# Kernel tuning notes

Hardware: AMD Instinct MI355X
Metric: run time of the kernel (lower is better)

Reference implementation:

```python
import jax, jax.numpy as jnp
import numpy as np

N = 100000   # nodes
E = 1600000  # edges
G = 1000     # graphs
S = 32       # state_dim
H = 128      # hidden_dim_message / hidden_dim_output
F = 1        # num_features (edge coulomb)
ROUNDS = 5
NEG_SLOPE = 0.01
LN_EPS = 1e-5


def _ln(x, g, b):
    m = jnp.mean(x, axis=-1, keepdims=True)
    v = jnp.var(x, axis=-1, keepdims=True)
    return (x - m) / jnp.sqrt(v + LN_EPS) * g + b


def _lrelu(x):
    return jnp.where(x >= 0, x, NEG_SLOPE * x)


def _kaiming(k, shape):
    # torch kaiming_normal_(mode='fan_out', nonlinearity='leaky_relu'); W stored [in,out]
    gain = np.sqrt(2.0 / (1.0 + NEG_SLOPE ** 2))
    std = gain / np.sqrt(shape[1])
    return jax.random.normal(k, shape, dtype=jnp.float32) * std


def setup_inputs() -> dict:
    key = jax.random.key(0)
    ks = jax.random.split(key, 10)
    return {
        'node_from': jax.random.randint(ks[0], (E,), 0, N),
        'node_to': jax.random.randint(ks[1], (E,), 0, N),
        'edge_coulomb': jax.random.normal(ks[2], (E, F), dtype=jnp.float32),
        'node_graph_index': jax.random.randint(ks[3], (N,), 0, G),
        'num_nodes': N,
        'num_graphs': G,
        # message_net params
        'W1': _kaiming(ks[4], (S + F, H)), 'b1': jnp.zeros((H,), jnp.float32),
        'g1': jnp.ones((H,), jnp.float32), 'be1': jnp.zeros((H,), jnp.float32),
        'W2': _kaiming(ks[5], (H, S)), 'b2': jnp.zeros((S,), jnp.float32),
        'g2': jnp.ones((S,), jnp.float32), 'be2': jnp.zeros((S,), jnp.float32),
        # output_net params
        'Wo1': _kaiming(ks[6], (S, H)), 'bo1': jnp.zeros((H,), jnp.float32),
        'go': jnp.ones((H,), jnp.float32), 'beo': jnp.zeros((H,), jnp.float32),
        'Wo2': _kaiming(ks[7], (H, 2)), 'bo2': jnp.zeros((2,), jnp.float32),
    }


def reference(node_from, node_to, edge_coulomb, node_graph_index, num_nodes, num_graphs,
              W1, b1, g1, be1, W2, b2, g2, be2, Wo1, bo1, go, beo, Wo2, bo2):
    state = jnp.zeros((num_nodes, S), dtype=edge_coulomb.dtype)
    for _ in range(ROUNDS):
        inp = jnp.concatenate([state[node_from], edge_coulomb], axis=1)  # [E, S+F]
        h = _lrelu(_ln(inp @ W1 + b1, g1, be1))                           # [E, H]
        msg = _lrelu(_ln(h @ W2 + b2, g2, be2))                           # [E, S]
        state = state + jax.ops.segment_sum(msg, node_to, num_segments=num_nodes)
    graph_state = jax.ops.segment_sum(state, node_graph_index, num_segments=num_graphs)  # [G, S]
    h = _lrelu(_ln(graph_state @ Wo1 + bo1, go, beo))
    ev = h @ Wo2 + bo2                                                    # [G, 2]
    mu = ev[:, :1]
    var = jax.nn.softplus(ev[:, 1:])
    return jnp.concatenate([mu, var], axis=1)
```

## Files before the change

### kernel.cpp

```cpp
#include <hip/hip_runtime.h>
#include <hip/hip_bf16.h>

#define NN 100000
#define NE 1600000
#define NG 1000
#define SS 32
#define HH 128
#define ROUNDS 5

constexpr float NEG = 0.01f;
constexpr float EPS = 1e-5f;

constexpr long al4(long x)  { return (x + 3) & ~3L; }
constexpr long al16(long x) { return (x + 15) & ~15L; }

constexpr long OFF_STATE = 0;
constexpr long OFF_GS    = OFF_STATE + (long)NN * SS;
constexpr long OFF_W1T   = OFF_GS + (long)NG * SS;
constexpr long OFF_B1    = OFF_W1T + HH * 33;
constexpr long OFF_G1    = OFF_B1 + HH;
constexpr long OFF_BE1   = OFF_G1 + HH;
constexpr long OFF_W2    = OFF_BE1 + HH;
constexpr long OFF_B2    = OFF_W2 + HH * SS;
constexpr long OFF_G2    = OFF_B2 + SS;
constexpr long OFF_BE2   = OFF_G2 + SS;
constexpr long OFF_WO1   = OFF_BE2 + SS;
constexpr long OFF_BO1   = OFF_WO1 + SS * HH;
constexpr long OFF_GO    = OFF_BO1 + HH;
constexpr long OFF_BEO   = OFF_GO + HH;
constexpr long OFF_WO2   = OFF_BEO + HH;
constexpr long OFF_BO2   = OFF_WO2 + HH * 2;
constexpr long OFF_W1L   = al4(OFF_BO2 + 2);
constexpr long OFF_WSC   = OFF_W1L + HH;
constexpr long OFF_W1B   = al4(OFF_WSC + 2);
constexpr long OFF_W2F   = OFF_W1B + 2048;
constexpr long OFF_WPK   = OFF_W2F + 2048;
constexpr long OFF_Z0P   = OFF_WPK + 192;
constexpr long W_END     = OFF_Z0P + 68;
constexpr long OFF_DELTA = al4(W_END);
constexpr long F_Z      = al4(W_END);
constexpr long F_START  = al4(F_Z + (long)NN * 68);
constexpr long F_CURSOR = F_START + NN + 4;
constexpr long F_SSTART = F_CURSOR + NN;
constexpr long F_SCUR   = F_SSTART + NN + 4;
constexpr long F_BSUM   = F_SCUR + NN;
constexpr long F_GDEG   = F_BSUM + 512;
constexpr long F_GSTART = F_GDEG + NG;
constexpr long F_GCUR   = F_GSTART + NG + 4;
constexpr long F_GLIST  = F_GCUR + NG;
constexpr long F_EPK    = al16(F_GLIST + NN);
constexpr long F_SP     = F_EPK + (long)NE * 2;
constexpr long F_MSG    = al16(F_SP + NE);
constexpr long F_RC     = F_MSG;
constexpr long WS_TOTAL = F_MSG + (long)NE * 16;
constexpr long WS_FALLBACK = OFF_DELTA + (long)NN * SS;
constexpr int  NBLK_N  = (NN + 255) / 256;
constexpr int  CHSHIFT_E = 19;
constexpr int  NCH_E     = (NE + (1 << CHSHIFT_E) - 1) >> CHSHIFT_E;
constexpr int  CHSHIFT_P = 20;
constexpr int  NCH_P     = (NE + (1 << CHSHIFT_P) - 1) >> CHSHIFT_P;

typedef float f32x4 __attribute__((ext_vector_type(4)));
typedef unsigned int u32x4 __attribute__((ext_vector_type(4)));
typedef short s16x8 __attribute__((ext_vector_type(8)));

__device__ __forceinline__ s16x8 as_s16x8(u32x4 u) {
    union { u32x4 a; s16x8 b; } c; c.a = u; return c.b;
}
__device__ __forceinline__ float bf2f(unsigned short u) {
    union { unsigned int i; float f; } v;
    v.i = ((unsigned int)u) << 16;
    return v.f;
}
__device__ __forceinline__ float lo_bf(unsigned int p) {
    union { unsigned int i; float f; } v; v.i = p << 16; return v.f;
}
__device__ __forceinline__ float hi_bf(unsigned int p) {
    union { unsigned int i; float f; } v; v.i = p & 0xFFFF0000u; return v.f;
}
__device__ __forceinline__ unsigned short f2bf(float f) {
    union { float f; unsigned int u; } x; x.f = f;
    return (unsigned short)((x.u + 0x7FFFu + ((x.u >> 16) & 1u)) >> 16);
}
__device__ __forceinline__ unsigned int pack_bf2(float a, float b) {
    return (unsigned int)f2bf(a) | ((unsigned int)f2bf(b) << 16);
}
#if defined(__has_builtin)
#if __has_builtin(__builtin_amdgcn_cvt_pk_bf16_f32)
#define HAVE_CVT_PK_BF16 1
#endif
#endif
__device__ __forceinline__ unsigned int cvt2bf(float a, float b) {
#ifdef HAVE_CVT_PK_BF16
    auto r = __builtin_amdgcn_cvt_pk_bf16_f32(a, b);
    unsigned int u; __builtin_memcpy(&u, &r, 4); return u;
#else
    return pack_bf2(a, b);
#endif
}
template <int CTRL>
__device__ __forceinline__ float ror_add(float x) {
    int v = __builtin_amdgcn_update_dpp(0, __float_as_int(x), CTRL, 0xF, 0xF, true);
    return x + __int_as_float(v);
}
__device__ __forceinline__ float row_reduce16(float x) {
    x = ror_add<0x121>(x);
    x = ror_add<0x122>(x);
    x = ror_add<0x124>(x);
    x = ror_add<0x128>(x);
    return x;
}
__device__ __forceinline__ int is_bf16(const void* g1raw) {
    return (((const unsigned int*)g1raw)[0] & 0xFFFFu) != 0u;
}
__device__ __forceinline__ float ldf(const void* p, long idx, int bf) {
    return bf ? bf2f(((const unsigned short*)p)[idx]) : ((const float*)p)[idx];
}

__global__ void prep_kernel(
    const void* __restrict__ W1,  const void* __restrict__ b1,
    const void* __restrict__ g1,  const void* __restrict__ be1,
    const void* __restrict__ W2,  const void* __restrict__ b2,
    const void* __restrict__ g2,  const void* __restrict__ be2,
    const void* __restrict__ Wo1, const void* __restrict__ bo1,
    const void* __restrict__ go,  const void* __restrict__ beo,
    const void* __restrict__ Wo2, const void* __restrict__ bo2,
    float* __restrict__ ws)
{
    const int bf = is_bf16(g1);
    long idx = (long)blockIdx.x * blockDim.x + threadIdx.x;
    if (idx < (long)NN * SS) { ws[OFF_STATE + idx] = 0.f; ws[OFF_DELTA + idx] = 0.f; }
    if (idx < (long)NG * SS) ws[OFF_GS + idx] = 0.f;
    if (idx < NN) { ((int*)(ws + F_CURSOR))[idx] = 0; ((int*)(ws + F_SCUR))[idx] = 0; }
    if (idx < NG) ((int*)(ws + F_GDEG))[idx] = 0;
    if (idx < 33 * HH) {
        int i = (int)(idx / HH), k = (int)(idx % HH);
        ws[OFF_W1T + (long)k * 33 + i] = ldf(W1, idx, bf);
    }
    if (idx < HH) {
        ws[OFF_B1  + idx] = ldf(b1,  idx, bf);
        ws[OFF_G1  + idx] = ldf(g1,  idx, bf);
        ws[OFF_BE1 + idx] = ldf(be1, idx, bf);
        ws[OFF_BO1 + idx] = ldf(bo1, idx, bf);
        ws[OFF_GO  + idx] = ldf(go,  idx, bf);
        ws[OFF_BEO + idx] = ldf(beo, idx, bf);
        ws[OFF_W1L + idx] = ldf(W1, (long)32 * HH + idx, bf);
    }
    if (idx == 0) {
        float sw = 0.f, sq = 0.f;
        float sb = 0.f, qb = 0.f, db = 0.f;
        for (int i = 0; i < HH; i++) {
            float w = ldf(W1, (long)32 * HH + i, bf);
            float x = ldf(b1, i, bf);
            sw += w; sq = fmaf(w, w, sq);
            sb += x; qb = fmaf(x, x, qb); db = fmaf(x, w, db);
        }
        ws[OFF_WSC] = sw; ws[OFF_WSC + 1] = sq;
        float* z0s = ws + OFF_Z0P + 64;
        z0s[0] = sb; z0s[1] = qb; z0s[2] = db; z0s[3] = 0.f;
    }
    if (idx < 64) {
        ((unsigned int*)(ws + OFF_Z0P))[idx] =
            cvt2bf(ldf(b1, 2 * idx, bf), ldf(b1, 2 * idx + 1, bf));
    }
    if (idx < HH * SS) ws[OFF_W2 + idx] = ldf(W2, idx, bf);
    if (idx < SS) {
        ws[OFF_B2  + idx] = ldf(b2,  idx, bf);
        ws[OFF_G2  + idx] = ldf(g2,  idx, bf);
        ws[OFF_BE2 + idx] = ldf(be2, idx, bf);
    }
    if (idx < SS * HH) ws[OFF_WO1 + idx] = ldf(Wo1, idx, bf);
    if (idx < HH * 2)  ws[OFF_WO2 + idx] = ldf(Wo2, idx, bf);
    if (idx < 2)       ws[OFF_BO2 + idx] = ldf(bo2, idx, bf);
    if (idx < 2048) {
        int w = (int)idx;
        int qq = w & 3, L = (w >> 2) & 63, t = (int)(w >> 8);
        int k0 = (L >> 4) * 8 + 2 * qq;
        int n  = t * 16 + (L & 15);
        ((unsigned int*)(ws + OFF_W1B))[w] =
            pack_bf2(ldf(W1, (long)k0 * HH + n, bf), ldf(W1, (long)(k0 + 1) * HH + n, bf));
    }
    if (idx < 2048) {
        int w = (int)idx;
        int qq = w & 3, L = (w >> 2) & 63, t2 = (w >> 8) & 1, ks = (int)(w >> 9);
        int k0 = ks * 32 + (L >> 4) * 8 + 2 * qq;
        int n  = t2 * 16 + (L & 15);
        float v0 = ldf(W2, (long)k0 * SS + n, bf);
        float v1 = ldf(W2, (long)(k0 + 1) * SS + n, bf);
        ((unsigned int*)(ws + OFF_W2F))[w] = pack_bf2(v0, v1);
    }
    if (idx < 192) {
        int w = (int)idx;
        int grp = w / 12, rem = w % 12, slot = rem >> 2, q = rem & 3;
        int ks = grp >> 2, quad = grp & 3;
        int n = ks * 32 + quad * 8 + 2 * q;
        float v0, v1;
        if (slot == 0)      { v0 = ldf(W1, (long)32 * HH + n, bf); v1 = ldf(W1, (long)32 * HH + n + 1, bf); }
        else if (slot == 1) { v0 = ldf(g1, n, bf);  v1 = ldf(g1, n + 1, bf); }
        else                { v0 = ldf(be1, n, bf); v1 = ldf(be1, n + 1, bf); }
        ((unsigned int*)(ws + OFF_WPK))[w] = pack_bf2(v0, v1);
    }
}

__global__ void fillseq_kernel(const int* __restrict__ nfrom, const int* __restrict__ nto,
                               const void* __restrict__ ec, const void* __restrict__ g1raw,
                               float* ws) {
    int e = blockIdx.x * 256 + threadIdx.x;
    if (e < NE) {
        int u = nfrom[e];
        int v = nto[e];
        float ecv = ldf(ec, e, is_bf16(g1raw));
        int drank = atomicAdd(&((int*)(ws + F_CURSOR))[v], 1);
        int srank = atomicAdd(&((int*)(ws + F_SCUR))[u], 1);
        union { float f; unsigned int i; } c; c.f = ecv;
        u32x4 o; o[0] = (unsigned int)u; o[1] = c.i; o[2] = (unsigned int)drank; o[3] = (unsigned int)srank;
        *(u32x4*)((unsigned int*)(ws + F_RC) + (long)e * 4) = o;
    }
}

__global__ void scan1_kernel(float* ws, long degOff, long startOff) {
    __shared__ int sh[256];
    int* deg   = (int*)(ws + degOff);
    int* start = (int*)(ws + startOff);
    int* bsum  = (int*)(ws + F_BSUM);
    int i = blockIdx.x * 256 + threadIdx.x;
    int x = (i < NN) ? deg[i] : 0;
    sh[threadIdx.x] = x;
    __syncthreads();
    for (int off = 1; off < 256; off <<= 1) {
        int t = (threadIdx.x >= off) ? sh[threadIdx.x - off] : 0;
        __syncthreads();
        sh[threadIdx.x] += t;
        __syncthreads();
    }
    int incl = sh[threadIdx.x];
    if (i < NN) start[i] = incl - x;
    if (threadIdx.x == 255) bsum[blockIdx.x] = incl;
}

__global__ void scan2p_kernel(float* ws) {
    __shared__ int sh[512];
    int* bsum = (int*)(ws + F_BSUM);
    int t = threadIdx.x;
    int x = (t < NBLK_N) ? bsum[t] : 0;
    sh[t] = x;
    __syncthreads();
    for (int off = 1; off < 512; off <<= 1) {
        int v = (t >= off) ? sh[t - off] : 0;
        __syncthreads();
        sh[t] += v;
        __syncthreads();
    }
    if (t < NBLK_N) bsum[t] = sh[t] - x;
}

__global__ void scan3_kernel(float* ws, long startOff) {
    int* start  = (int*)(ws + startOff);
    int* bsum   = (int*)(ws + F_BSUM);
    int i = blockIdx.x * 256 + threadIdx.x;
    if (i < NN) {
        start[i] += bsum[i >> 8];
        if (i == 0) start[NN] = NE;
    }
}

__global__ void epkc_kernel(float* ws, int chunk) {
    int e = blockIdx.x * 256 + threadIdx.x;
    if (e < NE) {
        u32x4 rc = *(const u32x4*)((const unsigned int*)(ws + F_RC) + (long)e * 4);
        int spos = ((const int*)(ws + F_SSTART))[rc[0]] + (int)rc[3];
        if ((spos >> CHSHIFT_E) == chunk) {
            uint2 o; o.x = rc[0]; o.y = rc[1];
            *(uint2*)((unsigned int*)(ws + F_EPK) + (long)spos * 2) = o;
        }
    }
}

__global__ void spc_kernel(const int* __restrict__ nto, float* ws, int chunk) {
    int e = blockIdx.x * 256 + threadIdx.x;
    if (e < NE) {
        u32x4 rc = *(const u32x4*)((const unsigned int*)(ws + F_RC) + (long)e * 4);
        int dpos = ((const int*)(ws + F_START))[nto[e]] + (int)rc[2];
        if ((dpos >> CHSHIFT_P) == chunk) {
            int spos = ((const int*)(ws + F_SSTART))[rc[0]] + (int)rc[3];
            ((int*)(ws + F_SP))[dpos] = spos;
        }
    }
}

__global__ void ghist_kernel(const int* __restrict__ gidx, float* ws) {
    int i = blockIdx.x * 256 + threadIdx.x;
    if (i < NN) atomicAdd(&((int*)(ws + F_GDEG))[gidx[i]], 1);
}

__global__ void gscan_kernel(float* ws) {
    __shared__ int sh[1024];
    int* deg   = (int*)(ws + F_GDEG);
    int* start = (int*)(ws + F_GSTART);
    int* cur   = (int*)(ws + F_GCUR);
    int t = threadIdx.x;
    int x = (t < NG) ? deg[t] : 0;
    sh[t] = x;
    __syncthreads();
    for (int off = 1; off < 1024; off <<= 1) {
        int v = (t >= off) ? sh[t - off] : 0;
        __syncthreads();
        sh[t] += v;
        __syncthreads();
    }
    if (t < NG) { start[t] = sh[t] - x; cur[t] = sh[t] - x; }
    if (t == 0) start[NG] = NN;
}

__global__ void gfill_kernel(const int* __restrict__ gidx, float* ws) {
    int i = blockIdx.x * 256 + threadIdx.x;
    if (i < NN) {
        int pos = atomicAdd(&((int*)(ws + F_GCUR))[gidx[i]], 1);
        ((int*)(ws + F_GLIST))[pos] = i;
    }
}

__global__ void z0_kernel(float* __restrict__ ws)
{
    long idx = (long)blockIdx.x * 256 + threadIdx.x;
    if (idx < (long)NN * 68) {
        int slot = (int)(idx % 68);
        ((unsigned int*)(ws + F_Z))[idx] = ((const unsigned int*)(ws + OFF_Z0P))[slot];
    }
}

__launch_bounds__(256)
__global__ void node_kernel(float* __restrict__ ws, int do_z)
{
    __shared__ unsigned short zl[4][16 * 136];
    __shared__ float stl[64 * 33];
    const long nbase = (long)blockIdx.x * 64;

    {
        int t = threadIdx.x;
        int vl = t >> 2, sub = t & 3;
        long v = nbase + vl;
        if (v < NN) {
            const int* start = (const int*)(ws + F_START);
            const int* SPp   = (const int*)(ws + F_SP);
            const u32x4* mb = (const u32x4*)(ws + F_MSG);
            int s0 = start[v], s1 = start[v + 1];
            float* st = ws + OFF_STATE + v * SS + sub * 8;
            float a0 = st[0], a1 = st[1], a2 = st[2], a3 = st[3];
            float a4 = st[4], a5 = st[5], a6 = st[6], a7 = st[7];
            int p = s0;
            for (; p + 3 < s1; p += 4) {
                int q0 = SPp[p], q1 = SPp[p + 1], q2 = SPp[p + 2], q3 = SPp[p + 3];
                u32x4 m0 = mb[(long)q0 * 4 + sub];
                u32x4 m1 = mb[(long)q1 * 4 + sub];
                u32x4 m2 = mb[(long)q2 * 4 + sub];
                u32x4 m3 = mb[(long)q3 * 4 + sub];
                a0 += lo_bf(m0[0]); a1 += hi_bf(m0[0]);
                a2 += lo_bf(m0[1]); a3 += hi_bf(m0[1]);
                a4 += lo_bf(m0[2]); a5 += hi_bf(m0[2]);
                a6 += lo_bf(m0[3]); a7 += hi_bf(m0[3]);
                a0 += lo_bf(m1[0]); a1 += hi_bf(m1[0]);
                a2 += lo_bf(m1[1]); a3 += hi_bf(m1[1]);
                a4 += lo_bf(m1[2]); a5 += hi_bf(m1[2]);
                a6 += lo_bf(m1[3]); a7 += hi_bf(m1[3]);
                a0 += lo_bf(m2[0]); a1 += hi_bf(m2[0]);
                a2 += lo_bf(m2[1]); a3 += hi_bf(m2[1]);
                a4 += lo_bf(m2[2]); a5 += hi_bf(m2[2]);
                a6 += lo_bf(m2[3]); a7 += hi_bf(m2[3]);
                a0 += lo_bf(m3[0]); a1 += hi_bf(m3[0]);
                a2 += lo_bf(m3[1]); a3 += hi_bf(m3[1]);
                a4 += lo_bf(m3[2]); a5 += hi_bf(m3[2]);
                a6 += lo_bf(m3[3]); a7 += hi_bf(m3[3]);
            }
            for (; p < s1; ++p) {
                int spv = SPp[p];
                u32x4 m = mb[(long)spv * 4 + sub];
                a0 += lo_bf(m[0]); a1 += hi_bf(m[0]);
                a2 += lo_bf(m[1]); a3 += hi_bf(m[1]);
                a4 += lo_bf(m[2]); a5 += hi_bf(m[2]);
                a6 += lo_bf(m[3]); a7 += hi_bf(m[3]);
            }
            st[0] = a0; st[1] = a1; st[2] = a2; st[3] = a3;
            st[4] = a4; st[5] = a5; st[6] = a6; st[7] = a7;
            float* sl = stl + vl * 33 + sub * 8;
            sl[0] = a0; sl[1] = a1; sl[2] = a2; sl[3] = a3;
            sl[4] = a4; sl[5] = a5; sl[6] = a6; sl[7] = a7;
        }
    }
    if (!do_z) return;
    __syncthreads();

    const int wv = threadIdx.x >> 6, lane = threadIdx.x & 63;
    const int col = lane & 15, quad = lane >> 4;
    const long vbase = nbase + wv * 16;
    if (vbase >= NN) return;

    const float* sl = stl + (wv * 16 + col) * 33 + quad * 8;
    float st[8];
#pragma unroll
    for (int j = 0; j < 8; j++) st[j] = sl[j];

    u32x4 au;
    au[0] = cvt2bf(st[0], st[1]);
    au[1] = cvt2bf(st[2], st[3]);
    au[2] = cvt2bf(st[4], st[5]);
    au[3] = cvt2bf(st[6], st[7]);
    s16x8 af = as_s16x8(au);

    const u32x4* W1B = (const u32x4*)(ws + OFF_W1B);
    const float* B1 = ws + OFF_B1;
    f32x4 acc[8];
#pragma unroll
    for (int t = 0; t < 8; t++) {
        float bb = B1[t * 16 + col];
        acc[t][0] = bb; acc[t][1] = bb; acc[t][2] = bb; acc[t][3] = bb;
        acc[t] = __builtin_amdgcn_mfma_f32_16x16x32_bf16(af, as_s16x8(W1B[t * 64 + lane]), acc[t], 0, 0, 0);
    }

    float s[4] = {0.f, 0.f, 0.f, 0.f}, q[4] = {0.f, 0.f, 0.f, 0.f}, d[4] = {0.f, 0.f, 0.f, 0.f};
    const float* W1L = ws + OFF_W1L;
#pragma unroll
    for (int t = 0; t < 8; t++) {
        float wl = W1L[t * 16 + col];
#pragma unroll
        for (int r = 0; r < 4; r++) {
            float z = acc[t][r];
            s[r] += z; q[r] = fmaf(z, z, q[r]); d[r] = fmaf(z, wl, d[r]);
        }
    }
#pragma unroll
    for (int r = 0; r < 4; r++) {
        float sr = row_reduce16(s[r]);
        float qr = row_reduce16(q[r]);
        float dr = row_reduce16(d[r]);
        if (col == 0) {
            f32x4 o; o[0] = sr; o[1] = qr; o[2] = dr; o[3] = 0.f;
            *(f32x4*)(ws + F_Z + (vbase + quad * 4 + r) * 68 + 64) = o;
        }
    }

    unsigned short* zw_ = zl[wv];
#pragma unroll
    for (int t = 0; t < 8; t++) {
        unsigned int p01 = cvt2bf(acc[t][0], acc[t][1]);
        unsigned int p23 = cvt2bf(acc[t][2], acc[t][3]);
        unsigned short* b = zw_ + quad * (4 * 136) + t * 16 + col;
        b[0]       = (unsigned short)p01;
        b[136]     = (unsigned short)(p01 >> 16);
        b[2 * 136] = (unsigned short)p23;
        b[3 * 136] = (unsigned short)(p23 >> 16);
    }
    unsigned int* zg = (unsigned int*)(ws + F_Z);
#pragma unroll
    for (int it = 0; it < 4; it++) {
        int byte = it * 1024 + lane * 16;
        int node = byte >> 8;
        int ko   = (byte & 255) >> 2;
        u32x4 val = *(const u32x4*)(zw_ + node * 136 + ((byte & 255) >> 1));
        *(u32x4*)(zg + (vbase + node) * 68L + ko) = val;
    }
}

__launch_bounds__(256)
__global__ void edge_src_kernel(float* __restrict__ ws)
{
    const int lane = threadIdx.x & 63, wv = threadIdx.x >> 6;
    const int col = lane & 15, quad = lane >> 4;

    const u32x4* W2Fp = (const u32x4*)(ws + OFF_W2F);
    u32x4 w2f[8];
#pragma unroll
    for (int i = 0; i < 8; i++) w2f[i] = W2Fp[i * 64 + lane];
    u32x4 wlp[4], gp[4], bep[4];
    const u32x4* WPKp = (const u32x4*)(ws + OFF_WPK);
#pragma unroll
    for (int ks = 0; ks < 4; ks++) {
        const u32x4* W = WPKp + (ks * 4 + quad) * 3;
        wlp[ks] = W[0]; gp[ks] = W[1]; bep[ks] = W[2];
    }
    f32x4 g2h[2], be2h[2], b2h[2];
#pragma unroll
    for (int t2 = 0; t2 < 2; t2++) {
        g2h[t2]  = *(const f32x4*)(ws + OFF_G2  + t2 * 16 + quad * 4);
        be2h[t2] = *(const f32x4*)(ws + OFF_BE2 + t2 * 16 + quad * 4);
        b2h[t2]  = *(const f32x4*)(ws + OFF_B2  + t2 * 16 + quad * 4);
    }
    const float sw1 = ws[OFF_WSC], sqw1 = ws[OFF_WSC + 1];

    const uint2* EPKp = (const uint2*)((const unsigned int*)(ws + F_EPK));
    const long tbase = ((long)blockIdx.x * 4 + wv) * 4;

    uint2 epk[4];
#pragma unroll
    for (int k = 0; k < 4; k++)
        epk[k] = EPKp[(tbase + k) * 16 + col];
    f32x4 zst[4];
#pragma unroll
    for (int k = 0; k < 4; k++)
        zst[k] = *(const f32x4*)(ws + F_Z + (long)(int)epk[k].x * 68 + 64);

#pragma unroll
    for (int k = 0; k < 4; k++) {
        const int epos = (int)((tbase + k) * 16) + col;
        const int u = (int)epk[k].x;
        union { unsigned int i; float f; } cc; cc.i = epk[k].y;
        const float ecv = cc.f;

        float sumh = fmaf(ecv, sw1, zst[k][0]);
        float sqh  = fmaf(ecv, fmaf(ecv, sqw1, 2.f * zst[k][2]), zst[k][1]);
        float mean = sumh * (1.f / HH);
        float var  = fmaxf(sqh * (1.f / HH) - mean * mean, 0.f);
        float inv  = rsqrtf(var + EPS);
        const float alpha = inv, beta = -mean * inv;

        const unsigned int* zrow = (const unsigned int*)(ws + F_Z) + (long)u * 68;
        u32x4 zw[4];
#pragma unroll
        for (int ks = 0; ks < 4; ks++)
            zw[ks] = *(const u32x4*)(zrow + ks * 16 + quad * 4);

        f32x4 acc2[2];
        acc2[0] = b2h[0]; acc2[1] = b2h[1];

#pragma unroll
        for (int ks = 0; ks < 4; ks++) {
            u32x4 zwv = zw[ks];
            u32x4 hu;
#pragma unroll
            for (int w = 0; w < 4; w++) {
                float z0 = lo_bf(zwv[w]), z1 = hi_bf(zwv[w]);
                float h0 = fmaf(ecv, lo_bf(wlp[ks][w]), z0);
                float h1 = fmaf(ecv, hi_bf(wlp[ks][w]), z1);
                h0 = fmaf(h0, alpha, beta);
                h1 = fmaf(h1, alpha, beta);
                h0 = fmaf(h0, lo_bf(gp[ks][w]), lo_bf(bep[ks][w]));
                h1 = fmaf(h1, hi_bf(gp[ks][w]), hi_bf(bep[ks][w]));
                h0 = fmaxf(h0, NEG * h0);
                h1 = fmaxf(h1, NEG * h1);
                hu[w] = cvt2bf(h0, h1);
            }
            s16x8 hf = as_s16x8(hu);
            acc2[0] = __builtin_amdgcn_mfma_f32_16x16x32_bf16(as_s16x8(w2f[ks * 2 + 0]), hf, acc2[0], 0, 0, 0);
            acc2[1] = __builtin_amdgcn_mfma_f32_16x16x32_bf16(as_s16x8(w2f[ks * 2 + 1]), hf, acc2[1], 0, 0, 0);
        }

        float s2 = 0.f, q2 = 0.f;
#pragma unroll
        for (int t2 = 0; t2 < 2; t2++)
#pragma unroll
            for (int r = 0; r < 4; r++) { float vv = acc2[t2][r]; s2 += vv; q2 = fmaf(vv, vv, q2); }
        s2 += __shfl_xor(s2, 16); q2 += __shfl_xor(q2, 16);
        s2 += __shfl_xor(s2, 32); q2 += __shfl_xor(q2, 32);
        float mean2 = s2 * (1.f / SS);
        float var2  = fmaxf(q2 * (1.f / SS) - mean2 * mean2, 0.f);
        float inv2  = rsqrtf(var2 + EPS);
        const float a2 = inv2, b2c = -mean2 * inv2;

        unsigned int* dst = (unsigned int*)(ws + F_MSG) + (long)epos * 16;
#pragma unroll
        for (int t2 = 0; t2 < 2; t2++) {
            float m0 = fmaf(fmaf(acc2[t2][0], a2, b2c), g2h[t2][0], be2h[t2][0]);
            float m1 = fmaf(fmaf(acc2[t2][1], a2, b2c), g2h[t2][1], be2h[t2][1]);
            float m2 = fmaf(fmaf(acc2[t2][2], a2, b2c), g2h[t2][2], be2h[t2][2]);
            float m3 = fmaf(fmaf(acc2[t2][3], a2, b2c), g2h[t2][3], be2h[t2][3]);
            m0 = fmaxf(m0, NEG * m0); m1 = fmaxf(m1, NEG * m1);
            m2 = fmaxf(m2, NEG * m2); m3 = fmaxf(m3, NEG * m3);
            uint2 o; o.x = cvt2bf(m0, m1); o.y = cvt2bf(m2, m3);
            *(uint2*)(dst + t2 * 8 + quad * 2) = o;
        }
    }
}

__launch_bounds__(256)
__global__ void graph_gather_kernel(float* __restrict__ ws)
{
    int t = blockIdx.x * 256 + threadIdx.x;
    int g = t >> 5;
    if (g >= NG) return;
    int j = t & 31;
    const int* start = (const int*)(ws + F_GSTART);
    const int* list  = (const int*)(ws + F_GLIST);
    int s0 = start[g], s1 = start[g + 1];
    float acc = 0.f;
    for (int p = s0; p < s1; ++p)
        acc += ws[OFF_STATE + (long)list[p] * SS + j];
    ws[OFF_GS + (long)g * SS + j] = acc;
}

__launch_bounds__(256)
__global__ void edge_atomic_kernel(const int* __restrict__ nfrom, const int* __restrict__ nto,
                                   const void* __restrict__ ec, const void* __restrict__ g1raw,
                                   const float* __restrict__ cws, float* delta)
{
    int e = blockIdx.x * 256 + threadIdx.x;
    if (e >= NE) return;
    const float* state = cws + OFF_STATE;
    const float* W1T = cws + OFF_W1T;
    const float* B1  = cws + OFF_B1;
    const float* G1  = cws + OFF_G1;
    const float* BE1 = cws + OFF_BE1;
    const float* W2  = cws + OFF_W2;
    const float* B2  = cws + OFF_B2;
    const float* G2  = cws + OFF_G2;
    const float* BE2 = cws + OFF_BE2;
    int u = nfrom[e];
    float inp[33];
    const float4* srow = (const float4*)(state + (long)u * SS);
#pragma unroll
    for (int i = 0; i < 8; i++) {
        float4 v = srow[i];
        inp[i * 4 + 0] = v.x; inp[i * 4 + 1] = v.y;
        inp[i * 4 + 2] = v.z; inp[i * 4 + 3] = v.w;
    }
    inp[32] = ldf(ec, e, is_bf16(g1raw));
    float sum = 0.f, sq = 0.f;
    for (int k = 0; k < HH; k++) {
        const float* wr = W1T + k * 33;
        float a = B1[k];
#pragma unroll
        for (int i = 0; i < 33; i++) a = fmaf(inp[i], wr[i], a);
        sum += a; sq = fmaf(a, a, sq);
    }
    float mean = sum * (1.f / HH);
    float var  = sq * (1.f / HH) - mean * mean;
    float inv  = rsqrtf(var + EPS);
    float msg[SS];
#pragma unroll
    for (int j = 0; j < SS; j++) msg[j] = B2[j];
    for (int k = 0; k < HH; k++) {
        const float* wr = W1T + k * 33;
        float a = B1[k];
#pragma unroll
        for (int i = 0; i < 33; i++) a = fmaf(inp[i], wr[i], a);
        float hk = fmaf((a - mean) * inv, G1[k], BE1[k]);
        hk = hk >= 0.f ? hk : NEG * hk;
        const float* w2r = W2 + k * SS;
#pragma unroll
        for (int j = 0; j < SS; j++) msg[j] = fmaf(hk, w2r[j], msg[j]);
    }
    float s2 = 0.f, q2 = 0.f;
#pragma unroll
    for (int j = 0; j < SS; j++) { s2 += msg[j]; q2 = fmaf(msg[j], msg[j], q2); }
    float m2 = s2 * (1.f / SS);
    float v2 = q2 * (1.f / SS) - m2 * m2;
    float i2 = rsqrtf(v2 + EPS);
    int v = nto[e];
    float* drow = delta + (long)v * SS;
#pragma unroll
    for (int j = 0; j < SS; j++) {
        float mj = fmaf((msg[j] - m2) * i2, G2[j], BE2[j]);
        mj = mj >= 0.f ? mj : NEG * mj;
        atomicAdd(drow + j, mj);
    }
}

__global__ void update_kernel(float* ws)
{
    long idx = (long)blockIdx.x * blockDim.x + threadIdx.x;
    if (idx < (long)NN * SS) {
        ws[OFF_STATE + idx] += ws[OFF_DELTA + idx];
        ws[OFF_DELTA + idx] = 0.f;
    }
}

__global__ void graph_kernel(const int* __restrict__ gidx, float* ws)
{
    long idx = (long)blockIdx.x * blockDim.x + threadIdx.x;
    if (idx < (long)NN * SS) {
        int i = (int)(idx >> 5);
        int j = (int)(idx & 31);
        atomicAdd(&ws[OFF_GS + (long)gidx[i] * SS + j], ws[OFF_STATE + idx]);
    }
}

__global__ void readout_kernel(const float* __restrict__ ws, const void* __restrict__ g1raw,
                               void* __restrict__ out)
{
    int g = blockIdx.x;
    int j = threadIdx.x;
    __shared__ float row[SS];
    __shared__ float buf[HH];
    __shared__ float p0[HH];
    __shared__ float p1[HH];

    const float* gs  = ws + OFF_GS;
    const float* Wo1 = ws + OFF_WO1;
    if (j < SS) row[j] = gs[(long)g * SS + j];
    __syncthreads();

    float a = ws[OFF_BO1 + j];
#pragma unroll
    for (int i = 0; i < SS; i++) a = fmaf(row[i], Wo1[i * HH + j], a);
    buf[j] = a;
    __syncthreads();

    float sum = 0.f, sq = 0.f;
    for (int i = 0; i < HH; i++) { float x = buf[i]; sum += x; sq = fmaf(x, x, sq); }
    float mean = sum * (1.f / HH);
    float var  = sq * (1.f / HH) - mean * mean;
    float inv  = rsqrtf(var + EPS);
    float h = fmaf((a - mean) * inv, ws[OFF_GO + j], ws[OFF_BEO + j]);
    h = h >= 0.f ? h : NEG * h;

    p0[j] = h * ws[OFF_WO2 + j * 2 + 0];
    p1[j] = h * ws[OFF_WO2 + j * 2 + 1];
    __syncthreads();

    if (j == 0) {
        float e0 = ws[OFF_BO2 + 0], e1 = ws[OFF_BO2 + 1];
        for (int i = 0; i < HH; i++) { e0 += p0[i]; e1 += p1[i]; }
        float sp = (e1 > 20.f) ? e1 : log1pf(expf(e1));
        if (is_bf16(g1raw)) {
            __hip_bfloat16* o = (__hip_bfloat16*)out;
            o[g * 2 + 0] = __float2bfloat16(e0);
            o[g * 2 + 1] = __float2bfloat16(sp);
        } else {
            float* o = (float*)out;
            o[g * 2 + 0] = e0;
            o[g * 2 + 1] = sp;
        }
    }
}

extern "C" void kernel_launch(void* const* d_in, const int* in_sizes, int n_in,
                              void* d_out, int out_size, void* d_ws, size_t ws_size,
                              hipStream_t stream)
{
    const int* nfrom = (const int*)d_in[0];
    const int* nto   = (const int*)d_in[1];
    const void* ec   = d_in[2];
    const int* gidx  = (const int*)d_in[3];
    const void* W1  = d_in[6];
    const void* b1  = d_in[7];
    const void* g1  = d_in[8];
    const void* be1 = d_in[9];
    const void* W2  = d_in[10];
    const void* b2  = d_in[11];
    const void* g2  = d_in[12];
    const void* be2 = d_in[13];
    const void* Wo1 = d_in[14];
    const void* bo1 = d_in[15];
    const void* go  = d_in[16];
    const void* beo = d_in[17];
    const void* Wo2 = d_in[18];
    const void* bo2 = d_in[19];

    float* ws = (float*)d_ws;
    if (ws_size < (size_t)WS_FALLBACK * sizeof(float)) return;
    const bool gather = ws_size >= (size_t)WS_TOTAL * sizeof(float);

    const int nsBlocks = (int)(((long)NN * SS + 255) / 256);
    const int eBlocks  = (NE + 255) / 256;
    const int efBlocks = NE / 256;
    const int ndBlocks = (NN + 63) / 64;
    const int z0Blocks = (int)(((long)NN * 68 + 255) / 256);
    const int nBlocks1 = (NN + 255) / 256;

    prep_kernel<<<nsBlocks, 256, 0, stream>>>(W1, b1, g1, be1, W2, b2, g2, be2,
                                              Wo1, bo1, go, beo, Wo2, bo2, ws);
    if (gather) {
        fillseq_kernel<<<eBlocks, 256, 0, stream>>>(nfrom, nto, ec, g1, ws);
        scan1_kernel<<<NBLK_N, 256, 0, stream>>>(ws, F_CURSOR, F_START);
        scan2p_kernel<<<1, 512, 0, stream>>>(ws);
        scan3_kernel<<<NBLK_N, 256, 0, stream>>>(ws, F_START);
        scan1_kernel<<<NBLK_N, 256, 0, stream>>>(ws, F_SCUR, F_SSTART);
        scan2p_kernel<<<1, 512, 0, stream>>>(ws);
        scan3_kernel<<<NBLK_N, 256, 0, stream>>>(ws, F_SSTART);
        for (int c = 0; c < NCH_E; c++)
            epkc_kernel<<<eBlocks, 256, 0, stream>>>(ws, c);
        for (int c = 0; c < NCH_P; c++)
            spc_kernel<<<eBlocks, 256, 0, stream>>>(nto, ws, c);
        ghist_kernel<<<nBlocks1, 256, 0, stream>>>(gidx, ws);
        gscan_kernel<<<1, 1024, 0, stream>>>(ws);
        gfill_kernel<<<nBlocks1, 256, 0, stream>>>(gidx, ws);
        z0_kernel<<<z0Blocks, 256, 0, stream>>>(ws);
        for (int r = 0; r < ROUNDS; r++) {
            edge_src_kernel<<<efBlocks, 256, 0, stream>>>(ws);
            node_kernel    <<<ndBlocks, 256, 0, stream>>>(ws, (r < ROUNDS - 1) ? 1 : 0);
        }
        graph_gather_kernel<<<(NG * 32 + 255) / 256, 256, 0, stream>>>(ws);
    } else {
        for (int r = 0; r < ROUNDS; r++) {
            edge_atomic_kernel<<<eBlocks, 256, 0, stream>>>(nfrom, nto, ec, g1, ws, ws + OFF_DELTA);
            update_kernel<<<nsBlocks, 256, 0, stream>>>(ws);
        }
        graph_kernel<<<nsBlocks, 256, 0, stream>>>(gidx, ws);
    }
    readout_kernel<<<NG, HH, 0, stream>>>(ws, g1, (void*)d_out);
}
```

Before: 1.158 ms.

## Slim preprocessing records, skip Z init via round-zero specialization, unroll gather by eight

```diff
diff --git a/kernel.cpp b/kernel.cpp
--- a/kernel.cpp
+++ b/kernel.cpp
@@ -203,18 +203,15 @@
 }
 
 __global__ void fillseq_kernel(const int* __restrict__ nfrom, const int* __restrict__ nto,
-                               const void* __restrict__ ec, const void* __restrict__ g1raw,
                                float* ws) {
     int e = blockIdx.x * 256 + threadIdx.x;
     if (e < NE) {
         int u = nfrom[e];
         int v = nto[e];
-        float ecv = ldf(ec, e, is_bf16(g1raw));
         int drank = atomicAdd(&((int*)(ws + F_CURSOR))[v], 1);
         int srank = atomicAdd(&((int*)(ws + F_SCUR))[u], 1);
-        union { float f; unsigned int i; } c; c.f = ecv;
-        u32x4 o; o[0] = (unsigned int)u; o[1] = c.i; o[2] = (unsigned int)drank; o[3] = (unsigned int)srank;
-        *(u32x4*)((unsigned int*)(ws + F_RC) + (long)e * 4) = o;
+        uint2 o; o.x = (unsigned int)drank; o.y = (unsigned int)srank;
+        *(uint2*)((unsigned int*)(ws + F_RC) + (long)e * 2) = o;
     }
 }
 
@@ -264,25 +261,29 @@
     }
 }
 
-__global__ void epkc_kernel(float* ws, int chunk) {
+__global__ void epkc_kernel(const int* __restrict__ nfrom, const void* __restrict__ ec,
+                            const void* __restrict__ g1raw, float* ws, int chunk) {
     int e = blockIdx.x * 256 + threadIdx.x;
     if (e < NE) {
-        u32x4 rc = *(const u32x4*)((const unsigned int*)(ws + F_RC) + (long)e * 4);
-        int spos = ((const int*)(ws + F_SSTART))[rc[0]] + (int)rc[3];
+        uint2 rc = *(const uint2*)((const unsigned int*)(ws + F_RC) + (long)e * 2);
+        int u = nfrom[e];
+        int spos = ((const int*)(ws + F_SSTART))[u] + (int)rc.y;
         if ((spos >> CHSHIFT_E) == chunk) {
-            uint2 o; o.x = rc[0]; o.y = rc[1];
+            union { float f; unsigned int i; } c; c.f = ldf(ec, e, is_bf16(g1raw));
+            uint2 o; o.x = (unsigned int)u; o.y = c.i;
             *(uint2*)((unsigned int*)(ws + F_EPK) + (long)spos * 2) = o;
         }
     }
 }
 
-__global__ void spc_kernel(const int* __restrict__ nto, float* ws, int chunk) {
+__global__ void spc_kernel(const int* __restrict__ nfrom, const int* __restrict__ nto,
+                           float* ws, int chunk) {
     int e = blockIdx.x * 256 + threadIdx.x;
     if (e < NE) {
-        u32x4 rc = *(const u32x4*)((const unsigned int*)(ws + F_RC) + (long)e * 4);
-        int dpos = ((const int*)(ws + F_START))[nto[e]] + (int)rc[2];
+        uint2 rc = *(const uint2*)((const unsigned int*)(ws + F_RC) + (long)e * 2);
+        int dpos = ((const int*)(ws + F_START))[nto[e]] + (int)rc.x;
         if ((dpos >> CHSHIFT_P) == chunk) {
-            int spos = ((const int*)(ws + F_SSTART))[rc[0]] + (int)rc[3];
+            int spos = ((const int*)(ws + F_SSTART))[nfrom[e]] + (int)rc.y;
             ((int*)(ws + F_SP))[dpos] = spos;
         }
     }
@@ -320,15 +321,6 @@
     }
 }
 
-__global__ void z0_kernel(float* __restrict__ ws)
-{
-    long idx = (long)blockIdx.x * 256 + threadIdx.x;
-    if (idx < (long)NN * 68) {
-        int slot = (int)(idx % 68);
-        ((unsigned int*)(ws + F_Z))[idx] = ((const unsigned int*)(ws + OFF_Z0P))[slot];
-    }
-}
-
 __launch_bounds__(256)
 __global__ void node_kernel(float* __restrict__ ws, int do_z)
 {
@@ -349,6 +341,50 @@
             float a0 = st[0], a1 = st[1], a2 = st[2], a3 = st[3];
             float a4 = st[4], a5 = st[5], a6 = st[6], a7 = st[7];
             int p = s0;
+            for (; p + 7 < s1; p += 8) {
+                int q0 = SPp[p],     q1 = SPp[p + 1], q2 = SPp[p + 2], q3 = SPp[p + 3];
+                int q4 = SPp[p + 4], q5 = SPp[p + 5], q6 = SPp[p + 6], q7 = SPp[p + 7];
+                u32x4 m0 = mb[(long)q0 * 4 + sub];
+                u32x4 m1 = mb[(long)q1 * 4 + sub];
+                u32x4 m2 = mb[(long)q2 * 4 + sub];
+                u32x4 m3 = mb[(long)q3 * 4 + sub];
+                u32x4 m4 = mb[(long)q4 * 4 + sub];
+                u32x4 m5 = mb[(long)q5 * 4 + sub];
+                u32x4 m6 = mb[(long)q6 * 4 + sub];
+                u32x4 m7 = mb[(long)q7 * 4 + sub];
+                a0 += lo_bf(m0[0]); a1 += hi_bf(m0[0]);
+                a2 += lo_bf(m0[1]); a3 += hi_bf(m0[1]);
+                a4 += lo_bf(m0[2]); a5 += hi_bf(m0[2]);
+                a6 += lo_bf(m0[3]); a7 += hi_bf(m0[3]);
+                a0 += lo_bf(m1[0]); a1 += hi_bf(m1[0]);
+                a2 += lo_bf(m1[1]); a3 += hi_bf(m1[1]);
+                a4 += lo_bf(m1[2]); a5 += hi_bf(m1[2]);
+                a6 += lo_bf(m1[3]); a7 += hi_bf(m1[3]);
+                a0 += lo_bf(m2[0]); a1 += hi_bf(m2[0]);
+                a2 += lo_bf(m2[1]); a3 += hi_bf(m2[1]);
+                a4 += lo_bf(m2[2]); a5 += hi_bf(m2[2]);
+                a6 += lo_bf(m2[3]); a7 += hi_bf(m2[3]);
+                a0 += lo_bf(m3[0]); a1 += hi_bf(m3[0]);
+                a2 += lo_bf(m3[1]); a3 += hi_bf(m3[1]);
+                a4 += lo_bf(m3[2]); a5 += hi_bf(m3[2]);
+                a6 += lo_bf(m3[3]); a7 += hi_bf(m3[3]);
+                a0 += lo_bf(m4[0]); a1 += hi_bf(m4[0]);
+                a2 += lo_bf(m4[1]); a3 += hi_bf(m4[1]);
+                a4 += lo_bf(m4[2]); a5 += hi_bf(m4[2]);
+                a6 += lo_bf(m4[3]); a7 += hi_bf(m4[3]);
+                a0 += lo_bf(m5[0]); a1 += hi_bf(m5[0]);
+                a2 += lo_bf(m5[1]); a3 += hi_bf(m5[1]);
+                a4 += lo_bf(m5[2]); a5 += hi_bf(m5[2]);
+                a6 += lo_bf(m5[3]); a7 += hi_bf(m5[3]);
+                a0 += lo_bf(m6[0]); a1 += hi_bf(m6[0]);
+                a2 += lo_bf(m6[1]); a3 += hi_bf(m6[1]);
+                a4 += lo_bf(m6[2]); a5 += hi_bf(m6[2]);
+                a6 += lo_bf(m6[3]); a7 += hi_bf(m6[3]);
+                a0 += lo_bf(m7[0]); a1 += hi_bf(m7[0]);
+                a2 += lo_bf(m7[1]); a3 += hi_bf(m7[1]);
+                a4 += lo_bf(m7[2]); a5 += hi_bf(m7[2]);
+                a6 += lo_bf(m7[3]); a7 += hi_bf(m7[3]);
+            }
             for (; p + 3 < s1; p += 4) {
                 int q0 = SPp[p], q1 = SPp[p + 1], q2 = SPp[p + 2], q3 = SPp[p + 3];
                 u32x4 m0 = mb[(long)q0 * 4 + sub];
@@ -461,6 +497,7 @@
     }
 }
 
+template <int R0>
 __launch_bounds__(256)
 __global__ void edge_src_kernel(float* __restrict__ ws)
 {
@@ -487,6 +524,15 @@
     }
     const float sw1 = ws[OFF_WSC], sqw1 = ws[OFF_WSC + 1];
 
+    f32x4 zst0;
+    u32x4 zw0[4];
+    if (R0) {
+        zst0 = *(const f32x4*)(ws + OFF_Z0P + 64);
+#pragma unroll
+        for (int ks = 0; ks < 4; ks++)
+            zw0[ks] = *(const u32x4*)((const unsigned int*)(ws + OFF_Z0P) + ks * 16 + quad * 4);
+    }
+
     const uint2* EPKp = (const uint2*)((const unsigned int*)(ws + F_EPK));
     const long tbase = ((long)blockIdx.x * 4 + wv) * 4;
 
@@ -495,9 +541,11 @@
     for (int k = 0; k < 4; k++)
         epk[k] = EPKp[(tbase + k) * 16 + col];
     f32x4 zst[4];
-#pragma unroll
-    for (int k = 0; k < 4; k++)
-        zst[k] = *(const f32x4*)(ws + F_Z + (long)(int)epk[k].x * 68 + 64);
+    if (!R0) {
+#pragma unroll
+        for (int k = 0; k < 4; k++)
+            zst[k] = *(const f32x4*)(ws + F_Z + (long)(int)epk[k].x * 68 + 64);
+    }
 
 #pragma unroll
     for (int k = 0; k < 4; k++) {
@@ -506,18 +554,24 @@
         union { unsigned int i; float f; } cc; cc.i = epk[k].y;
         const float ecv = cc.f;
 
-        float sumh = fmaf(ecv, sw1, zst[k][0]);
-        float sqh  = fmaf(ecv, fmaf(ecv, sqw1, 2.f * zst[k][2]), zst[k][1]);
+        f32x4 zs = R0 ? zst0 : zst[k];
+        float sumh = fmaf(ecv, sw1, zs[0]);
+        float sqh  = fmaf(ecv, fmaf(ecv, sqw1, 2.f * zs[2]), zs[1]);
         float mean = sumh * (1.f / HH);
         float var  = fmaxf(sqh * (1.f / HH) - mean * mean, 0.f);
         float inv  = rsqrtf(var + EPS);
         const float alpha = inv, beta = -mean * inv;
 
-        const unsigned int* zrow = (const unsigned int*)(ws + F_Z) + (long)u * 68;
         u32x4 zw[4];
-#pragma unroll
-        for (int ks = 0; ks < 4; ks++)
-            zw[ks] = *(const u32x4*)(zrow + ks * 16 + quad * 4);
+        if (R0) {
+#pragma unroll
+            for (int ks = 0; ks < 4; ks++) zw[ks] = zw0[ks];
+        } else {
+            const unsigned int* zrow = (const unsigned int*)(ws + F_Z) + (long)u * 68;
+#pragma unroll
+            for (int ks = 0; ks < 4; ks++)
+                zw[ks] = *(const u32x4*)(zrow + ks * 16 + quad * 4);
+        }
 
         f32x4 acc2[2];
         acc2[0] = b2h[0]; acc2[1] = b2h[1];
@@ -753,13 +807,12 @@
     const int eBlocks  = (NE + 255) / 256;
     const int efBlocks = NE / 256;
     const int ndBlocks = (NN + 63) / 64;
-    const int z0Blocks = (int)(((long)NN * 68 + 255) / 256);
     const int nBlocks1 = (NN + 255) / 256;
 
     prep_kernel<<<nsBlocks, 256, 0, stream>>>(W1, b1, g1, be1, W2, b2, g2, be2,
                                               Wo1, bo1, go, beo, Wo2, bo2, ws);
     if (gather) {
-        fillseq_kernel<<<eBlocks, 256, 0, stream>>>(nfrom, nto, ec, g1, ws);
+        fillseq_kernel<<<eBlocks, 256, 0, stream>>>(nfrom, nto, ws);
         scan1_kernel<<<NBLK_N, 256, 0, stream>>>(ws, F_CURSOR, F_START);
         scan2p_kernel<<<1, 512, 0, stream>>>(ws);
         scan3_kernel<<<NBLK_N, 256, 0, stream>>>(ws, F_START);
@@ -767,16 +820,16 @@
         scan2p_kernel<<<1, 512, 0, stream>>>(ws);
         scan3_kernel<<<NBLK_N, 256, 0, stream>>>(ws, F_SSTART);
         for (int c = 0; c < NCH_E; c++)
-            epkc_kernel<<<eBlocks, 256, 0, stream>>>(ws, c);
+            epkc_kernel<<<eBlocks, 256, 0, stream>>>(nfrom, ec, g1, ws, c);
         for (int c = 0; c < NCH_P; c++)
-            spc_kernel<<<eBlocks, 256, 0, stream>>>(nto, ws, c);
+            spc_kernel<<<eBlocks, 256, 0, stream>>>(nfrom, nto, ws, c);
         ghist_kernel<<<nBlocks1, 256, 0, stream>>>(gidx, ws);
         gscan_kernel<<<1, 1024, 0, stream>>>(ws);
         gfill_kernel<<<nBlocks1, 256, 0, stream>>>(gidx, ws);
-        z0_kernel<<<z0Blocks, 256, 0, stream>>>(ws);
         for (int r = 0; r < ROUNDS; r++) {
-            edge_src_kernel<<<efBlocks, 256, 0, stream>>>(ws);
-            node_kernel    <<<ndBlocks, 256, 0, stream>>>(ws, (r < ROUNDS - 1) ? 1 : 0);
+            if (r == 0) edge_src_kernel<1><<<efBlocks, 256, 0, stream>>>(ws);
+            else        edge_src_kernel<0><<<efBlocks, 256, 0, stream>>>(ws);
+            node_kernel<<<ndBlocks, 256, 0, stream>>>(ws, (r < ROUNDS - 1) ? 1 : 0);
         }
         graph_gather_kernel<<<(NG * 32 + 255) / 256, 256, 0, stream>>>(ws);
     } else {
```

Result: faster. 1.122 ms (-3.1%).
